# Performance work log

Measured on AMD Instinct MI355X. Metric: run time of the kernel, lower is better.

The kernel has to match this reference:

```python
import jax, jax.numpy as jnp
import numpy as np

N_RES = 500000


def _rot(vals):
    # stack 9 scalars-per-element into (..., 3, 3) row-major rotation matrices
    return jnp.stack(vals, axis=-1).reshape(*vals[0].shape, 3, 3)


def _dihedral(p0, p1, p2, p3):
    b0 = -(p1 - p0)
    b1 = p2 - p1
    b2 = p3 - p2
    b0xb1 = jnp.cross(b0, b1)
    b1xb2 = jnp.cross(b2, b1)
    y = jnp.sum(jnp.cross(b0xb1, b1xb2) * b1, axis=-1) / jnp.linalg.norm(b1, axis=-1)
    x = jnp.sum(b0xb1 * b1xb2, axis=-1)
    return jnp.nan_to_num(jnp.arctan2(y, x))


def _bb_dihedrals(N, CA, C):
    phi_ = _dihedral(C[:-1], N[1:], CA[1:], C[1:])
    psi_ = _dihedral(N[:-1], CA[:-1], C[:-1], N[1:])
    omg_ = _dihedral(CA[:-1], C[:-1], N[1:], CA[1:])
    pad = jnp.zeros_like(phi_[:1])
    omega = jnp.concatenate([omg_, pad])
    phi = jnp.concatenate([pad, phi_])
    psi = jnp.concatenate([psi_, pad])
    return jnp.stack([omega, phi, psi], axis=-1)  # (n, 3)


def _frames_from_reference(n_xyz, ca_xyz, c_xyz, eps=1e-20):
    # OpenFold Rigid.make_transform_from_reference
    n = n_xyz - ca_xyz
    c = c_xyz - ca_xyz
    cx, cy, cz = c[..., 0], c[..., 1], c[..., 2]
    z = jnp.zeros_like(cx)
    o = jnp.ones_like(cx)
    nrm = jnp.sqrt(eps + cx**2 + cy**2)
    s1, c1 = -cy / nrm, cx / nrm
    R1 = _rot([c1, -s1, z, s1, c1, z, z, z, o])
    nrm2 = jnp.sqrt(eps + cx**2 + cy**2 + cz**2)
    s2, c2 = cz / nrm2, jnp.sqrt(cx**2 + cy**2) / nrm2
    R2 = _rot([c2, z, s2, z, o, z, -s2, z, c2])
    Rc = R2 @ R1
    n2 = jnp.einsum('...ij,...j->...i', Rc, n)
    ny, nz_ = n2[..., 1], n2[..., 2]
    nrm3 = jnp.sqrt(eps + ny**2 + nz_**2)
    sn, cn = -nz_ / nrm3, ny / nrm3
    Rn = _rot([o, z, z, z, cn, -sn, z, sn, cn])
    rots = jnp.swapaxes(Rn @ Rc, -1, -2)
    return rots, ca_xyz  # (n,3,3), (n,3)


def _compose(ra, ta, rb, tb):
    # rigid composition: (ra,ta) o (rb,tb)
    return ra @ rb, jnp.einsum('...ij,...j->...i', ra, tb) + ta


def _forward(aa, bb_coords, sc_torsions, default_frames, group_idx, atom_mask, lit_positions):
    n_xyz, ca_xyz, c_xyz = bb_coords[:, 0], bb_coords[:, 1], bb_coords[:, 2]
    bb_r, bb_t = _frames_from_reference(n_xyz, ca_xyz, c_xyz)

    angles = jnp.concatenate([_bb_dihedrals(n_xyz, ca_xyz, c_xyz), sc_torsions], axis=-1)  # (n,7)
    alpha = jnp.stack([jnp.sin(angles), jnp.cos(angles)], axis=-1)  # (n,7,2) [sin, cos]
    bb_pad = jnp.concatenate([
        jnp.zeros((alpha.shape[0], 1, 1), alpha.dtype),
        jnp.ones((alpha.shape[0], 1, 1), alpha.dtype)], axis=-1)
    alpha = jnp.concatenate([bb_pad, alpha], axis=-2)  # (n,8,2)

    # torsion_angles_to_frames
    d4 = default_frames[aa]            # (n,8,4,4)
    dr, dt = d4[..., :3, :3], d4[..., :3, 3]
    s, cA = alpha[..., 0], alpha[..., 1]
    z = jnp.zeros_like(s)
    o = jnp.ones_like(s)
    Ra = _rot([o, z, z, z, cA, -s, z, s, cA])  # (n,8,3,3) x-axis rotation
    fr = dr @ Ra
    ft = dt
    # chain chi2->chi1, chi3->chi2, chi4->chi3
    r2, t2 = _compose(fr[:, 4], ft[:, 4], fr[:, 5], ft[:, 5])
    r3, t3 = _compose(r2, t2, fr[:, 6], ft[:, 6])
    r4, t4 = _compose(r3, t3, fr[:, 7], ft[:, 7])
    all_r = jnp.concatenate([fr[:, :5], r2[:, None], r3[:, None], r4[:, None]], axis=1)
    all_t = jnp.concatenate([ft[:, :5], t2[:, None], t3[:, None], t4[:, None]], axis=1)
    gr, gt = _compose(bb_r[:, None], bb_t[:, None], all_r, all_t)  # (n,8,3,3), (n,8,3)

    # frames_and_literature_positions_to_atom14_pos (one-hot sum == gather)
    n = aa.shape[0]
    g = group_idx[aa]                   # (n,14)
    ridx = jnp.arange(n)[:, None]
    ar = gr[ridx, g]                    # (n,14,3,3)
    at = gt[ridx, g]                    # (n,14,3)
    lit = lit_positions[aa]             # (n,14,3)
    pred = jnp.einsum('naij,naj->nai', ar, lit) + at
    pred = pred * atom_mask[aa][..., None]

    # use_native_bb_coords=True: keep input backbone atoms
    return jnp.concatenate([bb_coords, pred[:, 4:]], axis=1)  # (n,14,3)


def setup_inputs() -> dict:
    key = jax.random.key(0)
    ks = jax.random.split(key, 7)
    n = N_RES
    aa = jax.random.randint(ks[0], (n,), 0, 21, dtype=jnp.int32)
    bb_coords = jax.random.normal(ks[1], (n, 4, 3), jnp.float32) * 3.0
    sc_torsions = jax.random.uniform(ks[2], (n, 4), jnp.float32, -np.pi, np.pi)
    default_frames = jax.random.normal(ks[3], (21, 8, 4, 4), jnp.float32)
    group_idx = jax.random.randint(ks[4], (21, 14), 0, 8, dtype=jnp.int32)
    atom_mask = (jax.random.uniform(ks[5], (21, 14)) > 0.2).astype(jnp.float32)
    lit_positions = jax.random.normal(ks[6], (21, 14, 3), jnp.float32)
    return {"aa": aa, "bb_coords": bb_coords, "sc_torsions": sc_torsions,
            "default_frames": default_frames, "group_idx": group_idx,
            "atom_mask": atom_mask, "lit_positions": lit_positions}


def reference(aa, bb_coords, sc_torsions, default_frames, group_idx, atom_mask, lit_positions):
    return _forward(aa, bb_coords, sc_torsions, default_frames, group_idx, atom_mask, lit_positions)
```

## Files before the change

### kernel.cpp

```cpp
#include <hip/hip_runtime.h>
#include <hip/hip_fp16.h>


struct F3 { float x, y, z; };

__device__ __forceinline__ F3 f3sub(F3 a, F3 b) { return {a.x-b.x, a.y-b.y, a.z-b.z}; }
__device__ __forceinline__ F3 f3cross(F3 a, F3 b) {
    return {a.y*b.z - a.z*b.y, a.z*b.x - a.x*b.z, a.x*b.y - a.y*b.x};
}
__device__ __forceinline__ float f3dot(F3 a, F3 b) { return a.x*b.x + a.y*b.y + a.z*b.z; }

__device__ __forceinline__ void dihedral_from(F3 A, F3 B, F3 mid,
                                              float& s, float& c) {
    float x = f3dot(A, B);
    F3 w = f3cross(A, B);
    float y = f3dot(w, mid) * rsqrtf(fmaxf(f3dot(mid, mid), 1e-30f));
    float r2 = x * x + y * y;
    float rinv = rsqrtf(r2);
    bool ok = r2 > 1e-24f;
    s = ok ? y * rinv : 0.0f;
    c = ok ? x * rinv : 1.0f;
}

#define DF_AA     100
#define LIT_AA    34
#define OT_STRIDE 30

__global__ __launch_bounds__(256)
__attribute__((amdgpu_waves_per_eu(2, 4)))
void idealizer_kernel(
    const int*   __restrict__ aa,
    const float* __restrict__ bb,
    const float* __restrict__ tor,
    const float* __restrict__ dframes,
    const int*   __restrict__ gidx,
    const float* __restrict__ amask,
    const float* __restrict__ lit,
    float*       __restrict__ out,
    int n)
{
    __shared__ __align__(16) float  s_ot[256 * OT_STRIDE];
    __shared__ __align__(16) float  s_df[21 * DF_AA];
    __shared__ __align__(8)  __half s_lith[21 * LIT_AA];
    __shared__ unsigned s_gpk[21];
    __shared__ unsigned s_mbit[21];

    const int tid = threadIdx.x;
    for (int j = tid; j < 21 * 8 * 12; j += 256) {
        int blk = j / 12, e = j - blk * 12;
        s_df[(blk >> 3) * DF_AA + (blk & 7) * 12 + e] = dframes[blk * 16 + e];
    }
    for (int j = tid; j < 21 * 30; j += 256) {
        int a = j / 30, r = j - a * 30;
        s_lith[a * LIT_AA + r] = __float2half(lit[a * 42 + 12 + r]);
    }
    if (tid < 21) {
        unsigned gp = 0, mb = 0;
        #pragma unroll
        for (int a = 0; a < 10; a++) {
            gp |= ((unsigned)gidx[tid * 14 + 4 + a]) << (3 * a);
            mb |= (amask[tid * 14 + 4 + a] != 0.0f ? 1u : 0u) << a;
        }
        s_gpk[tid] = gp;
        s_mbit[tid] = mb;
    }
    __syncthreads();

    const int i0 = blockIdx.x * 256;
    const int i  = i0 + tid;
    if (i < n) {
        const int aai = aa[i];
        const float4* bb4 = (const float4*)bb;
        float4 q0 = bb4[i * 3 + 0];
        float4 q1 = bb4[i * 3 + 1];
        float Cz  = bb[i * 12 + 8];
        const int im = (i > 0)     ? i - 1 : 0;
        const int ip = (i < n - 1) ? i + 1 : 0;
        float4 t1 = bb4[im * 3 + 1];
        float  t2 = bb[im * 12 + 8];
        float4 r0 = bb4[ip * 3 + 0];
        float2 r1 = ((const float2*)bb)[ip * 6 + 2];
        float4 tv = ((const float4*)tor)[i];

        const unsigned gpk  = s_gpk[aai];
        const unsigned mbit = s_mbit[aai];
        float la[30];
        {
            const __half2* lh = (const __half2*)&s_lith[aai * LIT_AA];
            #pragma unroll
            for (int k = 0; k < 15; k++) {
                float2 t = __half22float2(lh[k]);
                la[2*k] = t.x; la[2*k+1] = t.y;
            }
        }
        const float* dfa = &s_df[aai * DF_AA];
        float4 nd0, nd1, nd2;
        {
            const float4* dfr = (const float4*)dfa;
            nd0 = dfr[0]; nd1 = dfr[1]; nd2 = dfr[2];
        }

        F3 Np  = {q0.x, q0.y, q0.z};
        F3 CAp = {q0.w, q1.x, q1.y};
        F3 Cp  = {q1.z, q1.w, Cz};
        F3 Cm  = {t1.z, t1.w, t2};
        F3 Nn  = {r0.x, r0.y, r0.z};
        F3 CAn = {r0.w, r1.x, r1.y};

        F3 u1 = f3sub(Np, Cm);
        F3 u2 = f3sub(CAp, Np);
        F3 u3 = f3sub(Cp, CAp);
        F3 u4 = f3sub(Nn, Cp);
        F3 u5 = f3sub(CAn, Nn);
        F3 c12 = f3cross(u1, u2), c23 = f3cross(u2, u3);
        F3 c34 = f3cross(u3, u4), c45 = f3cross(u4, u5);
        float s_ph, c_ph, s_ps, c_ps, s_om, c_om;
        dihedral_from(c12, c23, u2, s_ph, c_ph);
        dihedral_from(c23, c34, u3, s_ps, c_ps);
        dihedral_from(c34, c45, u4, s_om, c_om);
        if (i == 0)     { s_ph = 0.0f; c_ph = 1.0f; }
        if (i == n - 1) { s_ps = 0.0f; c_ps = 1.0f; s_om = 0.0f; c_om = 1.0f; }

        const float eps = 1e-20f;
        F3 nv = f3sub(Np, CAp);
        F3 cv = f3sub(Cp, CAp);
        float cx = cv.x, cy = cv.y, cz2 = cv.z;
        float d2xy  = cx * cx + cy * cy;
        float inrm  = rsqrtf(eps + d2xy);
        float s1 = -cy * inrm, c1 = cx * inrm;
        float inrm2 = rsqrtf(eps + d2xy + cz2 * cz2);
        float s2v = cz2 * inrm2, c2v = sqrtf(d2xy) * inrm2;
        float Rc00 = c2v * c1,  Rc01 = -c2v * s1, Rc02 = s2v;
        float Rc10 = s1,        Rc11 = c1,        Rc12 = 0.0f;
        float Rc20 = -s2v * c1, Rc21 = s2v * s1,  Rc22 = c2v;
        float n2y = Rc10 * nv.x + Rc11 * nv.y + Rc12 * nv.z;
        float n2z = Rc20 * nv.x + Rc21 * nv.y + Rc22 * nv.z;
        float inrm3 = rsqrtf(eps + n2y * n2y + n2z * n2z);
        float sn = -n2z * inrm3, cn = n2y * inrm3;
        float M10 = cn * Rc10 - sn * Rc20, M11 = cn * Rc11 - sn * Rc21, M12 = cn * Rc12 - sn * Rc22;
        float M20 = sn * Rc10 + cn * Rc20, M21 = sn * Rc11 + cn * Rc21;
        float M22 = sn * Rc12 + cn * Rc22;
        float B00 = Rc00, B01 = M10, B02 = M20;
        float B10 = Rc01, B11 = M11, B12 = M21;
        float B20 = Rc02, B21 = M12, B22 = M22;

        float sang[8], cang[8];
        sang[0] = 0.0f; cang[0] = 1.0f;
        sang[1] = s_om; cang[1] = c_om;
        sang[2] = s_ph; cang[2] = c_ph;
        sang[3] = s_ps; cang[3] = c_ps;
        __sincosf(tv.x, &sang[4], &cang[4]);
        __sincosf(tv.y, &sang[5], &cang[5]);
        __sincosf(tv.z, &sang[6], &cang[6]);
        __sincosf(tv.w, &sang[7], &cang[7]);

        float v[30];
        #pragma unroll
        for (int k = 0; k < 30; k++) v[k] = 0.0f;

        float L00, L01, L02, L10, L11, L12, L20, L21, L22, Lx, Ly, Lz;
        #pragma unroll
        for (int g = 0; g < 8; g++) {
            float4 d0 = nd0, d1 = nd1, d2 = nd2;
            if (g < 7) {
                const float4* dfr = (const float4*)(dfa + (g + 1) * 12);
                nd0 = dfr[0]; nd1 = dfr[1]; nd2 = dfr[2];
            }
            float sA = sang[g], cA = cang[g];
            float f00 = d0.x, f01 = cA * d0.y + sA * d0.z, f02 = cA * d0.z - sA * d0.y;
            float f10 = d1.x, f11 = cA * d1.y + sA * d1.z, f12 = cA * d1.z - sA * d1.y;
            float f20 = d2.x, f21 = cA * d2.y + sA * d2.z, f22 = cA * d2.z - sA * d2.y;
            if (g <= 4) {
                L00 = f00; L01 = f01; L02 = f02;
                L10 = f10; L11 = f11; L12 = f12;
                L20 = f20; L21 = f21; L22 = f22;
                Lx = d0.w; Ly = d1.w; Lz = d2.w;
            } else {
                float n00 = L00 * f00 + L01 * f10 + L02 * f20;
                float n01 = L00 * f01 + L01 * f11 + L02 * f21;
                float n02 = L00 * f02 + L01 * f12 + L02 * f22;
                float n10 = L10 * f00 + L11 * f10 + L12 * f20;
                float n11 = L10 * f01 + L11 * f11 + L12 * f21;
                float n12 = L10 * f02 + L11 * f12 + L12 * f22;
                float n20 = L20 * f00 + L21 * f10 + L22 * f20;
                float n21 = L20 * f01 + L21 * f11 + L22 * f21;
                float n22 = L20 * f02 + L21 * f12 + L22 * f22;
                float ntx = L00 * d0.w + L01 * d1.w + L02 * d2.w + Lx;
                float nty = L10 * d0.w + L11 * d1.w + L12 * d2.w + Ly;
                float ntz = L20 * d0.w + L21 * d1.w + L22 * d2.w + Lz;
                L00 = n00; L01 = n01; L02 = n02;
                L10 = n10; L11 = n11; L12 = n12;
                L20 = n20; L21 = n21; L22 = n22;
                Lx = ntx; Ly = nty; Lz = ntz;
            }

            #pragma unroll
            for (int a = 0; a < 10; a++) {
                bool sel = ((gpk >> (3 * a)) & 7u) == (unsigned)g;
                float qx = fmaf(L00, la[3*a], fmaf(L01, la[3*a+1], fmaf(L02, la[3*a+2], Lx)));
                float qy = fmaf(L10, la[3*a], fmaf(L11, la[3*a+1], fmaf(L12, la[3*a+2], Ly)));
                float qz = fmaf(L20, la[3*a], fmaf(L21, la[3*a+1], fmaf(L22, la[3*a+2], Lz)));
                v[3*a]   = sel ? qx : v[3*a];
                v[3*a+1] = sel ? qy : v[3*a+1];
                v[3*a+2] = sel ? qz : v[3*a+2];
            }
        }

        #pragma unroll
        for (int a = 0; a < 10; a++) {
            float mk = ((mbit >> a) & 1u) ? 1.0f : 0.0f;
            float qx = v[3*a], qy = v[3*a+1], qz = v[3*a+2];
            v[3*a]   = mk * fmaf(B00, qx, fmaf(B01, qy, fmaf(B02, qz, CAp.x)));
            v[3*a+1] = mk * fmaf(B10, qx, fmaf(B11, qy, fmaf(B12, qz, CAp.y)));
            v[3*a+2] = mk * fmaf(B20, qx, fmaf(B21, qy, fmaf(B22, qz, CAp.z)));
        }

        float2* so2 = (float2*)&s_ot[tid * OT_STRIDE];
        #pragma unroll
        for (int k = 0; k < 15; k++)
            so2[k] = make_float2(v[2*k], v[2*k+1]);
    }

    __syncthreads();

    int m = n - i0; if (m > 256) m = 256;
    float2* gout = (float2*)(out + (size_t)i0 * 42);
    const float2* bbt = (const float2*)(bb + (size_t)i0 * 12);
    if (m == 256) {
        int r = (tid * 24967) >> 19;
        int j = tid - r * 21;
        #pragma unroll
        for (int k = 0; k < 21; k++) {
            int off = tid + (k << 8);
            int bi = (j < 6) ? (r * 6 + j) : 0;
            float2 gval = bbt[bi];
            int tj = (j < 6) ? 0 : (j - 6);
            const float* tp = &s_ot[r * OT_STRIDE + 2 * tj];
            float2 lval = make_float2(tp[0], tp[1]);
            gout[off] = (j < 6) ? gval : lval;
            r += 12; j += 4;
            if (j >= 21) { j -= 21; r += 1; }
        }
    } else {
        const int cnt2 = m * 21;
        int r = tid / 21;
        int j = tid - r * 21;
        for (int off = tid; off < cnt2; off += 256) {
            int bi = (j < 6) ? (r * 6 + j) : 0;
            float2 gval = bbt[bi];
            int tj = (j < 6) ? 0 : (j - 6);
            const float* tp = &s_ot[r * OT_STRIDE + 2 * tj];
            float2 lval = make_float2(tp[0], tp[1]);
            gout[off] = (j < 6) ? gval : lval;
            r += 12; j += 4;
            if (j >= 21) { j -= 21; r += 1; }
        }
    }
}

extern "C" void kernel_launch(void* const* d_in, const int* in_sizes, int n_in,
                              void* d_out, int out_size, void* d_ws, size_t ws_size,
                              hipStream_t stream) {
    const int*   aa  = (const int*)d_in[0];
    const float* bb  = (const float*)d_in[1];
    const float* tor = (const float*)d_in[2];
    const float* df  = (const float*)d_in[3];
    const int*   gi  = (const int*)d_in[4];
    const float* am  = (const float*)d_in[5];
    const float* lp  = (const float*)d_in[6];
    float* outp = (float*)d_out;
    const int n = in_sizes[0];
    const int blocks = (n + 255) / 256;
    idealizer_kernel<<<blocks, 256, 0, stream>>>(aa, bb, tor, df, gi, am, lp, outp, n);
}
```

Measured before the change: 141.3 us.

## Precompute per-atom frame-literature products and evaluate atoms via chain-apply per group

Instead of building composed group frames for all 8 groups and evaluating every atom against each, the kernel precomputes per (residue type, atom) the default-frame times literature-position terms split into constant, cos and sin parts. Each atom is then computed directly from its group's sin/cos, which are looked up from shared memory, and is followed by conditional application of the chi frames F6, F5 and F4. This removes the 8x10 selected atom transforms and the frame-matrix chain products. The cost is that the U/V coefficients are stored in fp16, and frames 4-6 are loaded from global memory per thread.

```diff
diff --git a/kernel.cpp b/kernel.cpp
--- a/kernel.cpp
+++ b/kernel.cpp
@@ -22,9 +22,32 @@
     c = ok ? x * rinv : 1.0f;
 }
 
-#define DF_AA     100
-#define LIT_AA    34
-#define OT_STRIDE 30
+struct Xf12 { float m[9]; float t[3]; };
+__device__ __forceinline__ Xf12 mk_fr(float4 r0, float4 r1, float4 r2,
+                                      float sA, float cA) {
+    Xf12 o;
+    o.m[0] = r0.x; o.m[1] = fmaf(cA, r0.y, sA * r0.z); o.m[2] = fmaf(cA, r0.z, -sA * r0.y);
+    o.m[3] = r1.x; o.m[4] = fmaf(cA, r1.y, sA * r1.z); o.m[5] = fmaf(cA, r1.z, -sA * r1.y);
+    o.m[6] = r2.x; o.m[7] = fmaf(cA, r2.y, sA * r2.z); o.m[8] = fmaf(cA, r2.z, -sA * r2.y);
+    o.t[0] = r0.w; o.t[1] = r1.w; o.t[2] = r2.w;
+    return o;
+}
+
+__device__ __forceinline__ void cond_apply(const Xf12& F, bool cond,
+                                           float& qx, float& qy, float& qz) {
+    float tx = fmaf(F.m[0], qx, fmaf(F.m[1], qy, fmaf(F.m[2], qz, F.t[0])));
+    float ty = fmaf(F.m[3], qx, fmaf(F.m[4], qy, fmaf(F.m[5], qz, F.t[1])));
+    float tz = fmaf(F.m[6], qx, fmaf(F.m[7], qy, fmaf(F.m[8], qz, F.t[2])));
+    qx = cond ? tx : qx; qy = cond ? ty : qy; qz = cond ? tz : qz;
+}
+
+__device__ __forceinline__ float2 h2f(float packed) {
+    __half2 h = *reinterpret_cast<__half2*>(&packed);
+    return __half22float2(h);
+}
+
+#define OT_STRIDE 34
+#define AUV_AA    62
 
 __global__ __launch_bounds__(256)
 __attribute__((amdgpu_waves_per_eu(2, 4)))
@@ -39,20 +62,31 @@
     float*       __restrict__ out,
     int n)
 {
-    __shared__ __align__(16) float  s_ot[256 * OT_STRIDE];
-    __shared__ __align__(16) float  s_df[21 * DF_AA];
-    __shared__ __align__(8)  __half s_lith[21 * LIT_AA];
+    __shared__ __align__(16) float s_ot[256 * OT_STRIDE];
+    __shared__ __align__(16) float s_auv[21 * AUV_AA];
     __shared__ unsigned s_gpk[21];
     __shared__ unsigned s_mbit[21];
 
     const int tid = threadIdx.x;
-    for (int j = tid; j < 21 * 8 * 12; j += 256) {
-        int blk = j / 12, e = j - blk * 12;
-        s_df[(blk >> 3) * DF_AA + (blk & 7) * 12 + e] = dframes[blk * 16 + e];
-    }
-    for (int j = tid; j < 21 * 30; j += 256) {
-        int a = j / 30, r = j - a * 30;
-        s_lith[a * LIT_AA + r] = __float2half(lit[a * 42 + 12 + r]);
+
+    if (tid < 210) {
+        int aai = (tid * 6554) >> 16;
+        int a   = tid - aai * 10;
+        int g   = gidx[aai * 14 + 4 + a];
+        const float4* dr4 = (const float4*)dframes + (aai * 8 + g) * 4;
+        float4 d0 = dr4[0], d1 = dr4[1], d2 = dr4[2];
+        const float* lp = lit + aai * 42 + 12 + a * 3;
+        float lx = lp[0], ly = lp[1], lz = lp[2];
+        float* w = &s_auv[aai * AUV_AA + a * 6];
+        w[0] = fmaf(d0.x, lx, d0.w);
+        w[1] = fmaf(d1.x, lx, d1.w);
+        w[2] = fmaf(d2.x, lx, d2.w);
+        float U0 = fmaf(d0.y, ly, d0.z * lz), V0 = fmaf(d0.z, ly, -d0.y * lz);
+        float U1 = fmaf(d1.y, ly, d1.z * lz), V1 = fmaf(d1.z, ly, -d1.y * lz);
+        float U2 = fmaf(d2.y, ly, d2.z * lz), V2 = fmaf(d2.z, ly, -d2.y * lz);
+        ((__half2*)w)[3] = __floats2half2_rn(U0, U1);
+        ((__half2*)w)[4] = __floats2half2_rn(U2, V0);
+        ((__half2*)w)[5] = __floats2half2_rn(V1, V2);
     }
     if (tid < 21) {
         unsigned gp = 0, mb = 0;
@@ -81,24 +115,13 @@
         float4 r0 = bb4[ip * 3 + 0];
         float2 r1 = ((const float2*)bb)[ip * 6 + 2];
         float4 tv = ((const float4*)tor)[i];
+        const float4* dfp = (const float4*)dframes + (aai * 32 + 16);
+        float4 e40 = dfp[0], e41 = dfp[1],  e42 = dfp[2];
+        float4 e50 = dfp[4], e51 = dfp[5],  e52 = dfp[6];
+        float4 e60 = dfp[8], e61 = dfp[9],  e62 = dfp[10];
 
         const unsigned gpk  = s_gpk[aai];
         const unsigned mbit = s_mbit[aai];
-        float la[30];
-        {
-            const __half2* lh = (const __half2*)&s_lith[aai * LIT_AA];
-            #pragma unroll
-            for (int k = 0; k < 15; k++) {
-                float2 t = __half22float2(lh[k]);
-                la[2*k] = t.x; la[2*k+1] = t.y;
-            }
-        }
-        const float* dfa = &s_df[aai * DF_AA];
-        float4 nd0, nd1, nd2;
-        {
-            const float4* dfr = (const float4*)dfa;
-            nd0 = dfr[0]; nd1 = dfr[1]; nd2 = dfr[2];
-        }
 
         F3 Np  = {q0.x, q0.y, q0.z};
         F3 CAp = {q0.w, q1.x, q1.y};
@@ -154,68 +177,42 @@
         __sincosf(tv.z, &sang[6], &cang[6]);
         __sincosf(tv.w, &sang[7], &cang[7]);
 
+        float* row = &s_ot[tid * OT_STRIDE];
+        float2* scw = (float2*)(row + 18);
+        #pragma unroll
+        for (int g8 = 0; g8 < 8; g8++)
+            scw[g8] = make_float2(sang[g8], cang[g8]);
+
+        const Xf12 F4 = mk_fr(e40, e41, e42, sang[4], cang[4]);
+        const Xf12 F5 = mk_fr(e50, e51, e52, sang[5], cang[5]);
+        const Xf12 F6 = mk_fr(e60, e61, e62, sang[6], cang[6]);
+
         float v[30];
-        #pragma unroll
-        for (int k = 0; k < 30; k++) v[k] = 0.0f;
-
-        float L00, L01, L02, L10, L11, L12, L20, L21, L22, Lx, Ly, Lz;
-        #pragma unroll
-        for (int g = 0; g < 8; g++) {
-            float4 d0 = nd0, d1 = nd1, d2 = nd2;
-            if (g < 7) {
-                const float4* dfr = (const float4*)(dfa + (g + 1) * 12);
-                nd0 = dfr[0]; nd1 = dfr[1]; nd2 = dfr[2];
-            }
-            float sA = sang[g], cA = cang[g];
-            float f00 = d0.x, f01 = cA * d0.y + sA * d0.z, f02 = cA * d0.z - sA * d0.y;
-            float f10 = d1.x, f11 = cA * d1.y + sA * d1.z, f12 = cA * d1.z - sA * d1.y;
-            float f20 = d2.x, f21 = cA * d2.y + sA * d2.z, f22 = cA * d2.z - sA * d2.y;
-            if (g <= 4) {
-                L00 = f00; L01 = f01; L02 = f02;
-                L10 = f10; L11 = f11; L12 = f12;
-                L20 = f20; L21 = f21; L22 = f22;
-                Lx = d0.w; Ly = d1.w; Lz = d2.w;
-            } else {
-                float n00 = L00 * f00 + L01 * f10 + L02 * f20;
-                float n01 = L00 * f01 + L01 * f11 + L02 * f21;
-                float n02 = L00 * f02 + L01 * f12 + L02 * f22;
-                float n10 = L10 * f00 + L11 * f10 + L12 * f20;
-                float n11 = L10 * f01 + L11 * f11 + L12 * f21;
-                float n12 = L10 * f02 + L11 * f12 + L12 * f22;
-                float n20 = L20 * f00 + L21 * f10 + L22 * f20;
-                float n21 = L20 * f01 + L21 * f11 + L22 * f21;
-                float n22 = L20 * f02 + L21 * f12 + L22 * f22;
-                float ntx = L00 * d0.w + L01 * d1.w + L02 * d2.w + Lx;
-                float nty = L10 * d0.w + L11 * d1.w + L12 * d2.w + Ly;
-                float ntz = L20 * d0.w + L21 * d1.w + L22 * d2.w + Lz;
-                L00 = n00; L01 = n01; L02 = n02;
-                L10 = n10; L11 = n11; L12 = n12;
-                L20 = n20; L21 = n21; L22 = n22;
-                Lx = ntx; Ly = nty; Lz = ntz;
-            }
-
-            #pragma unroll
-            for (int a = 0; a < 10; a++) {
-                bool sel = ((gpk >> (3 * a)) & 7u) == (unsigned)g;
-                float qx = fmaf(L00, la[3*a], fmaf(L01, la[3*a+1], fmaf(L02, la[3*a+2], Lx)));
-                float qy = fmaf(L10, la[3*a], fmaf(L11, la[3*a+1], fmaf(L12, la[3*a+2], Ly)));
-                float qz = fmaf(L20, la[3*a], fmaf(L21, la[3*a+1], fmaf(L22, la[3*a+2], Lz)));
-                v[3*a]   = sel ? qx : v[3*a];
-                v[3*a+1] = sel ? qy : v[3*a+1];
-                v[3*a+2] = sel ? qz : v[3*a+2];
-            }
-        }
-
+        const float* auv = &s_auv[aai * AUV_AA];
         #pragma unroll
         for (int a = 0; a < 10; a++) {
+            int g = (gpk >> (3 * a)) & 7;
+            float2 sc = *(const float2*)(row + 18 + 2 * g);
+            const float* ap = auv + a * 6;
+            float2 w0 = *(const float2*)ap;
+            float2 w1 = *(const float2*)(ap + 2);
+            float2 w2 = *(const float2*)(ap + 4);
+            float2 u01  = h2f(w1.y);
+            float2 u2v0 = h2f(w2.x);
+            float2 v12  = h2f(w2.y);
+            float qx = fmaf(sc.y, u01.x,  fmaf(sc.x, u2v0.y, w0.x));
+            float qy = fmaf(sc.y, u01.y,  fmaf(sc.x, v12.x,  w0.y));
+            float qz = fmaf(sc.y, u2v0.x, fmaf(sc.x, v12.y,  w1.x));
+            cond_apply(F6, g >= 7, qx, qy, qz);
+            cond_apply(F5, g >= 6, qx, qy, qz);
+            cond_apply(F4, g >= 5, qx, qy, qz);
             float mk = ((mbit >> a) & 1u) ? 1.0f : 0.0f;
-            float qx = v[3*a], qy = v[3*a+1], qz = v[3*a+2];
             v[3*a]   = mk * fmaf(B00, qx, fmaf(B01, qy, fmaf(B02, qz, CAp.x)));
             v[3*a+1] = mk * fmaf(B10, qx, fmaf(B11, qy, fmaf(B12, qz, CAp.y)));
             v[3*a+2] = mk * fmaf(B20, qx, fmaf(B21, qy, fmaf(B22, qz, CAp.z)));
         }
 
-        float2* so2 = (float2*)&s_ot[tid * OT_STRIDE];
+        float2* so2 = (float2*)row;
         #pragma unroll
         for (int k = 0; k < 15; k++)
             so2[k] = make_float2(v[2*k], v[2*k+1]);
```

Result: faster. 137.3 us (-2.8%).
